# Kernel optimization log

Hardware: AMD Instinct MI355X
Metric: run time of the kernel (lower is better)

## Reference

```python
import jax, jax.numpy as jnp
import numpy as np

DIM = 256
FEATURE_SCALE = 4
NMS_THRESHOLD = 8.0
PRE_NMS_TOPK = 2048
MAX_OUTPUT = 256
MIN_SCORE = 0.2


def conv3d_same(x, w, b):
    # x: [D,H,W,Cin], w: [3,3,3,Cin,Cout] -> [D,H,W,Cout], SAME padding (flax default)
    y = jax.lax.conv_general_dilated(
        x[None], w, window_strides=(1, 1, 1), padding="SAME",
        dimension_numbers=("NDHWC", "DHWIO", "NDHWC"))
    return y[0] + b


def setup_inputs() -> dict:
    key = jax.random.key(0)
    ks = jax.random.split(key, 8)
    D, H, W, C = 16, 64, 64, 256
    feature = jax.random.normal(ks[0], (D, H, W, C), jnp.float32)
    mask = jax.random.bernoulli(ks[1], 0.8, (D * FEATURE_SCALE, H * FEATURE_SCALE, W * FEATURE_SCALE))
    s3a = 1.0 / np.sqrt(27 * C)
    s3b = 1.0 / np.sqrt(27 * DIM)
    s1 = 1.0 / np.sqrt(DIM)
    w0 = jax.random.normal(ks[2], (3, 3, 3, C, DIM), jnp.float32) * s3a
    b0 = jnp.zeros((DIM,), jnp.float32)
    w1 = jax.random.normal(ks[3], (3, 3, 3, DIM, DIM), jnp.float32) * s3b
    b1 = jnp.zeros((DIM,), jnp.float32)
    w_logit = jax.random.normal(ks[4], (DIM, 1), jnp.float32) * s1
    b_logit = jnp.zeros((1,), jnp.float32)
    w_reg = jax.random.normal(ks[5], (DIM, 3), jnp.float32) * s1
    b_reg = jnp.zeros((3,), jnp.float32)
    return dict(feature=feature, mask=mask, w0=w0, b0=b0, w1=w1, b1=b1,
                w_logit=w_logit, b_logit=b_logit, w_reg=w_reg, b_reg=b_reg)


def reference(feature, mask, w0, b0, w1, b1, w_logit, b_logit, w_reg, b_reg):
    # ---- feature mixing: n_layers=2 of conv3d + gelu (flax gelu is approximate/tanh) ----
    x = jax.nn.gelu(conv3d_same(feature, w0, b0))
    x = jax.nn.gelu(conv3d_same(x, w1, b1))
    D, H, W = x.shape[:3]

    # ---- detection block: 1x1 convs are pointwise dense layers ----
    logits = (x @ w_logit + b_logit)[..., 0].reshape(-1)          # [N]
    regressions = (x @ w_reg + b_reg)                              # [D,H,W,3]
    ref_locs = (jnp.moveaxis(jnp.mgrid[:D, :H, :W], 0, -1) + 0.5) * FEATURE_SCALE
    pred_locs = (ref_locs + regressions * FEATURE_SCALE).reshape(-1, 3)  # [N,3]

    # ---- generate_predictions: sigmoid scores, pre-NMS top-k, greedy distance NMS ----
    scores = jax.nn.sigmoid(logits)
    top_scores, idx = jax.lax.top_k(scores, PRE_NMS_TOPK)          # sorted desc
    top_locs = pred_locs[idx]                                      # [K,3]
    d2 = ((top_locs[:, None, :] - top_locs[None, :, :]) ** 2).sum(-1)  # [K,K]
    th2 = NMS_THRESHOLD * NMS_THRESHOLD

    def step(suppressed, i):
        keep_i = (~suppressed[i]) & (top_scores[i] >= MIN_SCORE)
        suppressed = suppressed | (keep_i & (d2[i] < th2))
        return suppressed, keep_i

    _, keep = jax.lax.scan(step, jnp.zeros((PRE_NMS_TOPK,), bool), jnp.arange(PRE_NMS_TOPK))
    sel_scores = jnp.where(keep, top_scores, 0.0)
    out_scores, oidx = jax.lax.top_k(sel_scores, MAX_OUTPUT)       # [M]
    out_locs = top_locs[oidx]                                      # [M,3]

    # ---- mask gather: floor/clip/index, zero out-of-mask scores ----
    pli = jnp.floor(out_locs).astype(jnp.int32)
    bound = jnp.array(mask.shape, jnp.int32) - 1
    plc = jnp.clip(pli, 0, bound)
    in_range = (pli == plc).all(axis=1)
    masked = jnp.where(in_range, mask[plc[:, 0], plc[:, 1], plc[:, 2]], False)
    out_scores = jnp.where(masked, out_scores, 0.0)

    return jnp.concatenate([out_locs, out_scores[:, None]], axis=-1)  # [M,4] = (z,y,x,score)
```

## Files before the change

### kernel.cpp

```cpp
#include <hip/hip_runtime.h>
#include <math.h>

#define Dz 16
#define Hy 64
#define Wx 64
#define CHN 256
#define NVOX (Dz*Hy*Wx)
#define TOPK 2048
#define MAXOUT 256
#define CAND_CAP 4096
#define NBCAP 16
#define NHIST 65536

typedef __attribute__((ext_vector_type(8))) _Float16 h8;
typedef __attribute__((ext_vector_type(8))) unsigned short u16x8;
typedef __attribute__((ext_vector_type(4))) float f32x4;

__device__ __forceinline__ float gelu_tanh(float x) {
    return 0.5f*x*(1.0f + tanhf(0.7978845608028654f*(x + 0.044715f*x*x*x)));
}
__device__ __forceinline__ unsigned f2sort(float f) {
    unsigned u = __float_as_uint(f);
    return (u & 0x80000000u) ? ~u : (u | 0x80000000u);
}
__device__ __forceinline__ float sort2f(unsigned s) {
    unsigned u = (s & 0x80000000u) ? (s & 0x7fffffffu) : ~s;
    return __uint_as_float(u);
}

#define MFMA(d, a, b) d = __builtin_amdgcn_mfma_f32_16x16x32_f16(a, b, d, 0, 0, 0)

__device__ __forceinline__ void gl_lds16(const void* g, void* l) {
    __builtin_amdgcn_global_load_lds(
        (const __attribute__((address_space(1))) void*)g,
        (__attribute__((address_space(3))) void*)l, 16, 0, 0);
}

__global__ __launch_bounds__(256) void prep_kernel(const float* __restrict__ w0,
        const float* __restrict__ w1, u16x8* __restrict__ wpk0,
        u16x8* __restrict__ wpk1, unsigned* __restrict__ hist,
        unsigned* __restrict__ counter, float4* __restrict__ zerob) {
    int b = blockIdx.x, t = threadIdx.x;
    if (b < 1728) {
        int id = b*256 + t;
        int l = (id >= 221184) ? 1 : 0;
        int r = id - l*221184;
        int lane = r & 63, ng = (r >> 6) & 15, kbg = (r >> 10) & 7, tp = r >> 13;
        const float* w = l ? w1 : w0;
        u16x8* dst = l ? wpk1 : wpk0;
        h8 hv, lv;
        #pragma unroll
        for (int j = 0; j < 8; ++j) {
            int k = kbg*32 + (lane >> 4)*8 + j;
            int co = ng*16 + (lane & 15);
            float v = w[((size_t)tp*CHN + k)*CHN + co];
            _Float16 h = (_Float16)v;
            hv[j] = h;
            lv[j] = (_Float16)(v - (float)h);
        }
        size_t base = (((size_t)(tp*8 + kbg)*16 + ng)*2)*64 + lane;
        dst[base]      = __builtin_bit_cast(u16x8, hv);
        dst[base + 64] = __builtin_bit_cast(u16x8, lv);
    } else {
        int zb = b - 1728;
        int i = zb*256 + t;
        hist[i] = 0u; hist[i + 16384] = 0u; hist[i + 32768] = 0u; hist[i + 49152] = 0u;
        if (zb == 0 && t == 0) counter[0] = 0u;
        if (zb == 0 && t == 2) *zerob = make_float4(0.f, 0.f, 0.f, 0.f);
    }
}

template<int LAYER>
__device__ __forceinline__ void stage_chunk(int cidx, void* ldst,
        const float* f32in, const unsigned short* hhi, const unsigned short* hlo,
        const float4* zerob, int zz, bool zok, int y0, int kc) {
    const void* src;
    if (LAYER == 0) {
        int c = cidx & 15, rr = cidx >> 4;
        int r = rr % 66, iy = rr / 66;
        int ygl = y0 - 1 + iy, xin = r - 1;
        bool ok = zok & ((unsigned)ygl < (unsigned)Hy) & ((unsigned)xin < (unsigned)Wx);
        int cs = c ^ ((r & 7) << 1);
        src = ok ? (const void*)(f32in + ((size_t)(((size_t)zz*Hy + ygl)*Wx + xin))*CHN
                                 + kc*64 + cs*4)
                 : (const void*)zerob;
    } else {
        int c = cidx & 7, rr = cidx >> 3;
        int r = rr % 66, tt = rr / 66;
        int p = tt >> 2, iy = tt & 3;
        int ygl = y0 - 1 + iy, xin = r - 1;
        bool ok = zok & ((unsigned)ygl < (unsigned)Hy) & ((unsigned)xin < (unsigned)Wx);
        int cs = c ^ (r & 7);
        const unsigned short* bp = p ? hlo : hhi;
        src = ok ? (const void*)(bp + ((size_t)(((size_t)zz*Hy + ygl)*Wx + xin))*CHN
                                 + kc*64 + cs*8)
                 : (const void*)zerob;
    }
    gl_lds16(src, ldst);
}

template<int LAYER>
__global__ __launch_bounds__(512, 4) void conv_kernel(
        const float* __restrict__ f32in,
        const unsigned short* __restrict__ hhi, const unsigned short* __restrict__ hlo,
        const u16x8* __restrict__ wpk, const float* __restrict__ bias,
        const float4* __restrict__ zerob,
        unsigned short* __restrict__ ohi, unsigned short* __restrict__ olo,
        const float* __restrict__ wlog, const float* __restrict__ blog,
        const float* __restrict__ wreg, const float* __restrict__ breg,
        float* __restrict__ locs, unsigned long long* __restrict__ keys,
        unsigned* __restrict__ hist) {
    __shared__ h8 sm[4224];
    const int tid = threadIdx.x;
    const int lane = tid & 63, w = tid >> 6;
    const int yo = w >> 2, wn = w & 3;
    const int lr = lane & 15, lg = lane >> 4;
    const int z = blockIdx.y, y0 = blockIdx.x*2;
    const int wbs = tid & ~63;

    f32x4 acc[4][4];
    #pragma unroll
    for (int m = 0; m < 4; ++m)
        #pragma unroll
        for (int n = 0; n < 4; ++n) acc[m][n] = (f32x4){0.f,0.f,0.f,0.f};

    for (int dz = 0; dz < 3; ++dz) {
        const int zz = z + dz - 1;
        const bool zok = (unsigned)zz < (unsigned)Dz;
        for (int kc = 0; kc < 4; ++kc) {
            __syncthreads();
            #pragma unroll
            for (int k = 0; k < 8; ++k)
                stage_chunk<LAYER>(k*512 + tid, (void*)&sm[k*512 + wbs],
                                   f32in, hhi, hlo, zerob, zz, zok, y0, kc);
            if (tid < 128)
                stage_chunk<LAYER>(4096 + tid, (void*)&sm[4096 + wbs],
                                   f32in, hhi, hlo, zerob, zz, zok, y0, kc);
            asm volatile("s_waitcnt vmcnt(0)" ::: "memory");
            __syncthreads();
            for (int dy = 0; dy < 3; ++dy) {
                const int iyA = yo + dy;
                #pragma unroll
                for (int dx = 0; dx < 3; ++dx) {
                    const int tap = (dz*3 + dy)*3 + dx;
                    #pragma unroll
                    for (int kb = 0; kb < 2; ++kb) {
                        const int kbg = kc*2 + kb;
                        const u16x8* wb = wpk + ((size_t)(tap*8 + kbg)*32 + wn*8)*64 + lane;
                        h8 bh[4];
                        #pragma unroll
                        for (int n = 0; n < 4; ++n)
                            bh[n] = __builtin_bit_cast(h8, wb[(size_t)n*128]);
                        #pragma unroll
                        for (int m = 0; m < 4; ++m) {
                            const int r = m*16 + lr + dx;
                            h8 ah, al;
                            if (LAYER == 0) {
                                const f32x4* Af = (const f32x4*)sm + ((size_t)iyA*66 + r)*16;
                                int s0 = (kb*8 + lg*2) ^ ((r & 7) << 1);
                                f32x4 a0 = Af[s0], a1 = Af[s0 | 1];
                                #pragma unroll
                                for (int j = 0; j < 4; ++j) {
                                    _Float16 h0 = (_Float16)a0[j];
                                    ah[j] = h0; al[j] = (_Float16)(a0[j] - (float)h0);
                                    _Float16 h1 = (_Float16)a1[j];
                                    ah[4+j] = h1; al[4+j] = (_Float16)(a1[j] - (float)h1);
                                }
                            } else {
                                const int sl = (kb*4 + lg) ^ (r & 7);
                                ah = sm[((size_t)iyA*66 + r)*8 + sl];
                                al = sm[2112 + ((size_t)iyA*66 + r)*8 + sl];
                            }
                            #pragma unroll
                            for (int n = 0; n < 4; ++n) {
                                MFMA(acc[m][n], ah, bh[n]);
                                MFMA(acc[m][n], al, bh[n]);
                            }
                        }
                        h8 bl[4];
                        #pragma unroll
                        for (int n = 0; n < 4; ++n)
                            bl[n] = __builtin_bit_cast(h8, wb[(size_t)n*128 + 64]);
                        #pragma unroll
                        for (int m = 0; m < 4; ++m) {
                            const int r = m*16 + lr + dx;
                            h8 ah;
                            if (LAYER == 0) {
                                const f32x4* Af = (const f32x4*)sm + ((size_t)iyA*66 + r)*16;
                                int s0 = (kb*8 + lg*2) ^ ((r & 7) << 1);
                                f32x4 a0 = Af[s0], a1 = Af[s0 | 1];
                                #pragma unroll
                                for (int j = 0; j < 4; ++j) {
                                    ah[j] = (_Float16)a0[j];
                                    ah[4+j] = (_Float16)a1[j];
                                }
                            } else {
                                const int sl = (kb*4 + lg) ^ (r & 7);
                                ah = sm[((size_t)iyA*66 + r)*8 + sl];
                            }
                            #pragma unroll
                            for (int n = 0; n < 4; ++n) MFMA(acc[m][n], ah, bl[n]);
                        }
                    }
                }
            }
        }
    }

    float bn[4];
    #pragma unroll
    for (int n = 0; n < 4; ++n) bn[n] = bias[wn*64 + n*16 + lr];

    if (LAYER == 0) {
        const int ygl = y0 + yo;
        #pragma unroll
        for (int m = 0; m < 4; ++m) {
            #pragma unroll
            for (int rg = 0; rg < 4; ++rg) {
                const int x = m*16 + lg*4 + rg;
                const size_t vbase = ((size_t)((z*Hy + ygl)*Wx + x))*CHN;
                #pragma unroll
                for (int n = 0; n < 4; ++n) {
                    const int co = wn*64 + n*16 + lr;
                    float g = gelu_tanh(acc[m][n][rg] + bn[n]);
                    _Float16 h = (_Float16)g;
                    _Float16 l = (_Float16)(g - (float)h);
                    ohi[vbase + co] = __builtin_bit_cast(unsigned short, h);
                    olo[vbase + co] = __builtin_bit_cast(unsigned short, l);
                }
            }
        }
    } else {
        float wl[4], wr0[4], wr1[4], wr2[4];
        #pragma unroll
        for (int n = 0; n < 4; ++n) {
            const int co = wn*64 + n*16 + lr;
            wl[n] = wlog[co];
            wr0[n] = wreg[co*3 + 0]; wr1[n] = wreg[co*3 + 1]; wr2[n] = wreg[co*3 + 2];
        }
        float p[4][16];
        #pragma unroll
        for (int c = 0; c < 4; ++c)
            #pragma unroll
            for (int xi = 0; xi < 16; ++xi) p[c][xi] = 0.f;
        #pragma unroll
        for (int m = 0; m < 4; ++m)
            #pragma unroll
            for (int rg = 0; rg < 4; ++rg) {
                const int xi = m*4 + rg;
                #pragma unroll
                for (int n = 0; n < 4; ++n) {
                    float g = gelu_tanh(acc[m][n][rg] + bn[n]);
                    p[0][xi] += g*wl[n];
                    p[1][xi] += g*wr0[n];
                    p[2][xi] += g*wr1[n];
                    p[3][xi] += g*wr2[n];
                }
            }
        #pragma unroll
        for (int st = 0; st < 4; ++st) {
            const int s = 1 << st;
            #pragma unroll
            for (int c = 0; c < 4; ++c)
                #pragma unroll
                for (int xi = 0; xi < 16; ++xi)
                    p[c][xi] += __shfl_xor(p[c][xi], s, 64);
        }
        __syncthreads();
        float* det = (float*)sm;
        if (lr == 0) {
            #pragma unroll
            for (int m = 0; m < 4; ++m)
                #pragma unroll
                for (int rg = 0; rg < 4; ++rg) {
                    const int x = m*16 + lg*4 + rg;
                    #pragma unroll
                    for (int c = 0; c < 4; ++c)
                        det[((yo*64 + x)*4 + c)*4 + wn] = p[c][m*4 + rg];
                }
        }
        __syncthreads();
        {
            const int yo2 = tid >> 8, x = (tid >> 2) & 63, chn = tid & 3;
            const float* dp = det + ((yo2*64 + x)*4 + chn)*4;
            float s = dp[0] + dp[1] + dp[2] + dp[3];
            const int ygl = y0 + yo2;
            const int vg = (z*Hy + ygl)*Wx + x;
            if (chn == 0) {
                float logit = s + blog[0];
                float score = 1.f/(1.f + expf(-logit));
                unsigned sb = f2sort(score);
                keys[vg] = ((unsigned long long)sb << 32)
                         | (unsigned long long)(0xFFFFFFFFu - (unsigned)vg);
                atomicAdd(&hist[sb >> 16], 1u);
            } else {
                float coord = (chn == 1) ? (float)z : (chn == 2) ? (float)ygl : (float)x;
                float loc = (coord + 0.5f)*4.0f + (s + breg[chn-1])*4.0f;
                locs[(size_t)vg*3 + (chn-1)] = loc;
            }
        }
    }
}

__global__ __launch_bounds__(1024) void find_cut_kernel(const unsigned* __restrict__ hist,
                                                        unsigned* __restrict__ cutp) {
    __shared__ unsigned ps[1024];
    __shared__ unsigned fs[64];
    __shared__ int sh_cb;
    __shared__ unsigned sh_acc;
    int t = threadIdx.x;
    unsigned s = 0;
    const unsigned* hp = hist + (size_t)t*64;
    for (int j = 0; j < 64; ++j) s += hp[j];
    ps[t] = s;
    __syncthreads();
    for (int off = 1; off < 1024; off <<= 1) {
        unsigned v = ps[t] + ((t + off < 1024) ? ps[t + off] : 0u);
        __syncthreads();
        ps[t] = v;
        __syncthreads();
    }
    if (ps[t] >= TOPK && (t == 1023 || ps[t+1] < TOPK)) {
        sh_cb = t; sh_acc = (t == 1023) ? 0u : ps[t+1];
    }
    __syncthreads();
    int cb = sh_cb; unsigned acc = sh_acc;
    if (t < 64) {
        unsigned f = acc;
        for (int u = t; u < 64; ++u) f += hist[(size_t)cb*64 + u];
        fs[t] = f;
    }
    __syncthreads();
    if (t < 64) {
        if (fs[t] >= TOPK && (t == 63 || fs[t+1] < TOPK))
            cutp[0] = ((unsigned)(cb*64 + t)) << 16;
    }
}

__global__ void compact_kernel(const unsigned long long* __restrict__ keys,
                               const unsigned* __restrict__ cutp,
                               unsigned* __restrict__ counter,
                               unsigned long long* __restrict__ cand) {
    int i = blockIdx.x*blockDim.x + threadIdx.x;
    unsigned thr = cutp[0];
    unsigned long long k = keys[i];
    if ((unsigned)(k >> 32) >= thr) {
        unsigned p = atomicAdd(counter, 1u);
        if (p < CAND_CAP) cand[p] = k;
    }
}

__global__ __launch_bounds__(128) void rank_kernel(const unsigned* __restrict__ counter,
        const unsigned long long* __restrict__ cand, const float* __restrict__ locs,
        float4* __restrict__ loc4G) {
    __shared__ unsigned long long kbuf[CAND_CAP];
    int t = threadIdx.x;
    int g = blockIdx.x*128 + t;
    int M = (int)*counter; if (M > CAND_CAP) M = CAND_CAP;
    for (int i = t; i < CAND_CAP; i += 128) kbuf[i] = (i < M) ? cand[i] : 0ull;
    __syncthreads();
    if (g >= M) return;
    unsigned long long mykey = kbuf[g];
    int rank = 0;
    for (int j = 0; j < M; ++j) rank += (kbuf[j] > mykey) ? 1 : 0;
    if (rank < TOPK) {
        unsigned idx = 0xFFFFFFFFu - (unsigned)(mykey & 0xFFFFFFFFull);
        float4 v;
        v.x = locs[(size_t)idx*3 + 0];
        v.y = locs[(size_t)idx*3 + 1];
        v.z = locs[(size_t)idx*3 + 2];
        v.w = sort2f((unsigned)(mykey >> 32));
        loc4G[rank] = v;
    }
}

__global__ __launch_bounds__(64) void nbr_kernel(const float4* __restrict__ loc4G,
        unsigned short* __restrict__ nbidx, unsigned char* __restrict__ nbcnt) {
    __shared__ float4 b4[TOPK];
    int t = threadIdx.x;
    int g = blockIdx.x*64 + t;
    for (int i = t; i < TOPK; i += 64) b4[i] = loc4G[i];
    __syncthreads();
    float4 me = b4[g];
    int cnt = 0;
    for (int j = 0; j < TOPK; ++j) {
        float4 o = b4[j];
        float dz = o.x - me.x, dy = o.y - me.y, dx = o.z - me.z;
        float d2 = dz*dz + dy*dy + dx*dx;
        if (d2 < 64.0f && j != g) {
            if (cnt < NBCAP) nbidx[(size_t)g*NBCAP + cnt] = (unsigned short)j;
            cnt++;
        }
    }
    nbcnt[g] = (unsigned char)min(cnt, 255);
}

__global__ __launch_bounds__(512) void nms_kernel(const float4* __restrict__ loc4G,
        const unsigned short* __restrict__ nbidx, const unsigned char* __restrict__ nbcnt,
        const int* __restrict__ mask, float* __restrict__ out) {
    __shared__ float4 p4[TOPK];
    __shared__ unsigned short snb[TOPK*NBCAP];
    __shared__ unsigned char scnt[TOPK];
    __shared__ unsigned char supf[TOPK];
    __shared__ unsigned char keepB[TOPK];
    __shared__ unsigned keepw[64];
    __shared__ int wpre[64];
    __shared__ int sh_nk;
    int t = threadIdx.x;
    for (int i = t; i < TOPK; i += 512) {
        p4[i] = loc4G[i]; scnt[i] = nbcnt[i]; supf[i] = 0; keepB[i] = 0;
    }
    for (int i = t; i < TOPK*NBCAP/8; i += 512)
        ((uint4*)snb)[i] = ((const uint4*)nbidx)[i];
    __syncthreads();
    if (t < 64) {
        const int l = t;
        float cz[32], cy[32], cx[32];
        #pragma unroll
        for (int j = 0; j < 32; ++j) {
            float4 v = p4[l*32 + j];
            cz[j] = v.x; cy[j] = v.y; cx[j] = v.z;
        }
        int myok = 0;
        #pragma unroll
        for (int j = 0; j < 32; ++j) myok += (p4[l*32 + j].w >= 0.2f) ? 1 : 0;
        #pragma unroll
        for (int s = 1; s < 64; s <<= 1) myok += __shfl_xor(myok, s, 64);
        const int NS = myok;
        int keeps = 0;
        for (int i = 0; i < NS; ++i) {
            bool kept = (supf[i] == 0);
            if (kept) {
                if (l == 0) keepB[i] = 1;
                ++keeps;
                const int cnt = scnt[i];
                if (cnt <= NBCAP) {
                    if (l < cnt) supf[snb[i*NBCAP + l]] = 1;
                } else {
                    float4 pv = p4[i];
                    #pragma unroll
                    for (int j = 0; j < 32; ++j) {
                        float dz = cz[j]-pv.x, dy = cy[j]-pv.y, dx = cx[j]-pv.z;
                        if (dz*dz + dy*dy + dx*dx < 64.0f) supf[l*32 + j] = 1;
                    }
                }
                asm volatile("s_waitcnt lgkmcnt(0)" ::: "memory");
                if (keeps >= MAXOUT) break;
            }
        }
    }
    __syncthreads();
    if (t < 64) {
        unsigned wmask = 0u;
        for (int j = 0; j < 32; ++j) wmask |= (keepB[t*32 + j] ? 1u : 0u) << j;
        keepw[t] = wmask;
    }
    __syncthreads();
    if (t < 64) {
        int p = 0;
        for (int j = 0; j < t; ++j) p += __popc(keepw[j]);
        wpre[t] = p;
        if (t == 63) sh_nk = p + __popc(keepw[63]);
    }
    __syncthreads();
    const int nk = sh_nk;
    for (int i = t; i < TOPK; i += 512) {
        unsigned w = keepw[i >> 5];
        bool kp = (w >> (i & 31)) & 1u;
        int rk = wpre[i >> 5] + __popc(w & ((1u << (i & 31)) - 1u));
        int slot = kp ? rk : (nk + (i - rk));
        if (slot < MAXOUT) {
            float4 v = p4[i];
            float lz = v.x, ly = v.y, lx = v.z;
            float sc = kp ? v.w : 0.f;
            int iz = (int)floorf(lz), iy = (int)floorf(ly), ix = (int)floorf(lx);
            int cz2 = min(max(iz,0),Dz*4-1), cy2 = min(max(iy,0),Hy*4-1), cx2 = min(max(ix,0),Wx*4-1);
            bool inr = (iz==cz2) && (iy==cy2) && (ix==cx2);
            float osc = (inr && mask[((size_t)cz2*(Hy*4) + cy2)*(Wx*4) + cx2] != 0) ? sc : 0.f;
            out[slot*4+0] = lz; out[slot*4+1] = ly; out[slot*4+2] = lx; out[slot*4+3] = osc;
        }
    }
}

extern "C" void kernel_launch(void* const* d_in, const int* in_sizes, int n_in,
                              void* d_out, int out_size, void* d_ws, size_t ws_size,
                              hipStream_t stream) {
    const float* feature = (const float*)d_in[0];
    const int*   mask    = (const int*)d_in[1];
    const float* w0   = (const float*)d_in[2];
    const float* b0   = (const float*)d_in[3];
    const float* w1   = (const float*)d_in[4];
    const float* b1   = (const float*)d_in[5];
    const float* wlog = (const float*)d_in[6];
    const float* blog = (const float*)d_in[7];
    const float* wreg = (const float*)d_in[8];
    const float* breg = (const float*)d_in[9];

    char* ws = (char*)d_ws;
    size_t off = 0;
    unsigned short* h1hi = (unsigned short*)(ws + off); off += (size_t)NVOX*CHN*2;
    unsigned short* h1lo = (unsigned short*)(ws + off); off += (size_t)NVOX*CHN*2;
    u16x8* wpk0 = (u16x8*)(ws + off);               off += (size_t)442368*16;
    u16x8* wpk1 = (u16x8*)(ws + off);               off += (size_t)442368*16;
    unsigned long long* keys = (unsigned long long*)(ws + off); off += (size_t)NVOX*8;
    float* locs = (float*)(ws + off);               off += (size_t)NVOX*3*4;
    unsigned* hist = (unsigned*)(ws + off);         off += (size_t)NHIST*4;
    unsigned* counter = (unsigned*)(ws + off);      off += 256;
    unsigned* cutp = counter + 1;
    float4* zerob = (float4*)(ws + off);            off += 256;
    unsigned long long* cand = (unsigned long long*)(ws + off); off += (size_t)CAND_CAP*8;
    float4* loc4G = (float4*)(ws + off);            off += (size_t)TOPK*16;
    unsigned short* nbidx = (unsigned short*)(ws + off); off += (size_t)TOPK*NBCAP*2;
    unsigned char* nbcnt = (unsigned char*)(ws + off);   off += (size_t)TOPK;
    if (ws_size < off) return;

    prep_kernel<<<1792, 256, 0, stream>>>(w0, w1, wpk0, wpk1, hist, counter, zerob);
    dim3 cgrid(Hy/2, Dz);
    conv_kernel<0><<<cgrid, 512, 0, stream>>>(feature, nullptr, nullptr, wpk0, b0,
                                              zerob, h1hi, h1lo,
                                              nullptr, nullptr, nullptr, nullptr,
                                              nullptr, nullptr, nullptr);
    conv_kernel<1><<<cgrid, 512, 0, stream>>>(nullptr, h1hi, h1lo, wpk1, b1,
                                              zerob, nullptr, nullptr,
                                              wlog, blog, wreg, breg,
                                              locs, keys, hist);
    find_cut_kernel<<<1, 1024, 0, stream>>>(hist, cutp);
    compact_kernel<<<NVOX/256, 256, 0, stream>>>(keys, cutp, counter, cand);
    rank_kernel<<<CAND_CAP/128, 128, 0, stream>>>(counter, cand, locs, loc4G);
    nbr_kernel<<<TOPK/64, 64, 0, stream>>>(loc4G, nbidx, nbcnt);
    nms_kernel<<<1, 512, 0, stream>>>(loc4G, nbidx, nbcnt, mask, (float*)d_out);
}
```

Before: 1.560 ms.

## Stage conv tiles via register loads and pre-split fp32 input into fp16 hi/lo

Replaces the direct global-to-LDS async loads with ordinary global loads into registers, then stores to shared memory with zero-fill for padding, which removes the need for the zero buffer. For layer 0 the fp32 input is split into fp16 hi/lo once during staging, so it is no longer reconverted for every tap and column in the inner MFMA loop. This cuts redundant conversion ALU work and lets both layers share one LDS read path. The cost is losing the async direct-to-LDS copy, so staging now goes through VGPRs and may add register pressure and latency.

```diff
diff --git a/kernel.cpp b/kernel.cpp
--- a/kernel.cpp
+++ b/kernel.cpp
@@ -30,16 +30,10 @@
 
 #define MFMA(d, a, b) d = __builtin_amdgcn_mfma_f32_16x16x32_f16(a, b, d, 0, 0, 0)
 
-__device__ __forceinline__ void gl_lds16(const void* g, void* l) {
-    __builtin_amdgcn_global_load_lds(
-        (const __attribute__((address_space(1))) void*)g,
-        (__attribute__((address_space(3))) void*)l, 16, 0, 0);
-}
-
 __global__ __launch_bounds__(256) void prep_kernel(const float* __restrict__ w0,
         const float* __restrict__ w1, u16x8* __restrict__ wpk0,
         u16x8* __restrict__ wpk1, unsigned* __restrict__ hist,
-        unsigned* __restrict__ counter, float4* __restrict__ zerob) {
+        unsigned* __restrict__ counter) {
     int b = blockIdx.x, t = threadIdx.x;
     if (b < 1728) {
         int id = b*256 + t;
@@ -66,45 +60,14 @@
         int i = zb*256 + t;
         hist[i] = 0u; hist[i + 16384] = 0u; hist[i + 32768] = 0u; hist[i + 49152] = 0u;
         if (zb == 0 && t == 0) counter[0] = 0u;
-        if (zb == 0 && t == 2) *zerob = make_float4(0.f, 0.f, 0.f, 0.f);
-    }
-}
-
-template<int LAYER>
-__device__ __forceinline__ void stage_chunk(int cidx, void* ldst,
-        const float* f32in, const unsigned short* hhi, const unsigned short* hlo,
-        const float4* zerob, int zz, bool zok, int y0, int kc) {
-    const void* src;
-    if (LAYER == 0) {
-        int c = cidx & 15, rr = cidx >> 4;
-        int r = rr % 66, iy = rr / 66;
-        int ygl = y0 - 1 + iy, xin = r - 1;
-        bool ok = zok & ((unsigned)ygl < (unsigned)Hy) & ((unsigned)xin < (unsigned)Wx);
-        int cs = c ^ ((r & 7) << 1);
-        src = ok ? (const void*)(f32in + ((size_t)(((size_t)zz*Hy + ygl)*Wx + xin))*CHN
-                                 + kc*64 + cs*4)
-                 : (const void*)zerob;
-    } else {
-        int c = cidx & 7, rr = cidx >> 3;
-        int r = rr % 66, tt = rr / 66;
-        int p = tt >> 2, iy = tt & 3;
-        int ygl = y0 - 1 + iy, xin = r - 1;
-        bool ok = zok & ((unsigned)ygl < (unsigned)Hy) & ((unsigned)xin < (unsigned)Wx);
-        int cs = c ^ (r & 7);
-        const unsigned short* bp = p ? hlo : hhi;
-        src = ok ? (const void*)(bp + ((size_t)(((size_t)zz*Hy + ygl)*Wx + xin))*CHN
-                                 + kc*64 + cs*8)
-                 : (const void*)zerob;
-    }
-    gl_lds16(src, ldst);
+    }
 }
 
 template<int LAYER>
 __global__ __launch_bounds__(512, 4) void conv_kernel(
-        const float* __restrict__ f32in,
+        const float* __restrict__ fsrc,
         const unsigned short* __restrict__ hhi, const unsigned short* __restrict__ hlo,
         const u16x8* __restrict__ wpk, const float* __restrict__ bias,
-        const float4* __restrict__ zerob,
         unsigned short* __restrict__ ohi, unsigned short* __restrict__ olo,
         const float* __restrict__ wlog, const float* __restrict__ blog,
         const float* __restrict__ wreg, const float* __restrict__ breg,
@@ -116,7 +79,6 @@
     const int yo = w >> 2, wn = w & 3;
     const int lr = lane & 15, lg = lane >> 4;
     const int z = blockIdx.y, y0 = blockIdx.x*2;
-    const int wbs = tid & ~63;
 
     f32x4 acc[4][4];
     #pragma unroll
@@ -126,20 +88,54 @@
 
     for (int dz = 0; dz < 3; ++dz) {
         const int zz = z + dz - 1;
-        const bool zok = (unsigned)zz < (unsigned)Dz;
         for (int kc = 0; kc < 4; ++kc) {
             __syncthreads();
-            #pragma unroll
-            for (int k = 0; k < 8; ++k)
-                stage_chunk<LAYER>(k*512 + tid, (void*)&sm[k*512 + wbs],
-                                   f32in, hhi, hlo, zerob, zz, zok, y0, kc);
-            if (tid < 128)
-                stage_chunk<LAYER>(4096 + tid, (void*)&sm[4096 + wbs],
-                                   f32in, hhi, hlo, zerob, zz, zok, y0, kc);
-            asm volatile("s_waitcnt vmcnt(0)" ::: "memory");
+            if (LAYER == 0) {
+                for (int cidx = tid; cidx < 2112; cidx += 512) {
+                    int cd = cidx & 7;
+                    int rr = cidx >> 3;
+                    int r = rr % 66, iy = rr / 66;
+                    int ygl = y0 - 1 + iy, xin = r - 1;
+                    h8 hv = {0,0,0,0,0,0,0,0}, lv = {0,0,0,0,0,0,0,0};
+                    if (((unsigned)zz < (unsigned)Dz) & ((unsigned)ygl < (unsigned)Hy)
+                        & ((unsigned)xin < (unsigned)Wx)) {
+                        const float* s = fsrc + ((size_t)((zz*Hy + ygl)*Wx + xin))*CHN
+                                              + kc*64 + cd*8;
+                        float4 t0 = *(const float4*)s;
+                        float4 t1 = *(const float4*)(s + 4);
+                        float vv[8] = {t0.x,t0.y,t0.z,t0.w,t1.x,t1.y,t1.z,t1.w};
+                        #pragma unroll
+                        for (int j = 0; j < 8; ++j) {
+                            _Float16 h = (_Float16)vv[j];
+                            hv[j] = h;
+                            lv[j] = (_Float16)(vv[j] - (float)h);
+                        }
+                    }
+                    int sl = cd ^ (r & 7);
+                    sm[(iy*66 + r)*8 + sl] = hv;
+                    sm[2112 + (iy*66 + r)*8 + sl] = lv;
+                }
+            } else {
+                for (int cidx = tid; cidx < 4224; cidx += 512) {
+                    int c = cidx & 7;
+                    int rr = cidx >> 3;
+                    int r = rr % 66, tt = rr / 66;
+                    int p = tt >> 2, iy = tt & 3;
+                    int ygl = y0 - 1 + iy, xin = r - 1;
+                    u16x8 v = {0,0,0,0,0,0,0,0};
+                    if (((unsigned)zz < (unsigned)Dz) & ((unsigned)ygl < (unsigned)Hy)
+                        & ((unsigned)xin < (unsigned)Wx)) {
+                        const unsigned short* bp = p ? hlo : hhi;
+                        v = *(const u16x8*)(bp + ((size_t)((zz*Hy + ygl)*Wx + xin))*CHN
+                                               + kc*64 + (size_t)((c ^ (r & 7)))*8);
+                    }
+                    sm[cidx] = __builtin_bit_cast(h8, v);
+                }
+            }
             __syncthreads();
             for (int dy = 0; dy < 3; ++dy) {
                 const int iyA = yo + dy;
+                const h8* As = sm + iyA*528;
                 #pragma unroll
                 for (int dx = 0; dx < 3; ++dx) {
                     const int tap = (dz*3 + dy)*3 + dx;
@@ -154,23 +150,9 @@
                         #pragma unroll
                         for (int m = 0; m < 4; ++m) {
                             const int r = m*16 + lr + dx;
-                            h8 ah, al;
-                            if (LAYER == 0) {
-                                const f32x4* Af = (const f32x4*)sm + ((size_t)iyA*66 + r)*16;
-                                int s0 = (kb*8 + lg*2) ^ ((r & 7) << 1);
-                                f32x4 a0 = Af[s0], a1 = Af[s0 | 1];
-                                #pragma unroll
-                                for (int j = 0; j < 4; ++j) {
-                                    _Float16 h0 = (_Float16)a0[j];
-                                    ah[j] = h0; al[j] = (_Float16)(a0[j] - (float)h0);
-                                    _Float16 h1 = (_Float16)a1[j];
-                                    ah[4+j] = h1; al[4+j] = (_Float16)(a1[j] - (float)h1);
-                                }
-                            } else {
-                                const int sl = (kb*4 + lg) ^ (r & 7);
-                                ah = sm[((size_t)iyA*66 + r)*8 + sl];
-                                al = sm[2112 + ((size_t)iyA*66 + r)*8 + sl];
-                            }
+                            const int sl = (kb*4 + lg) ^ (r & 7);
+                            h8 ah = As[r*8 + sl];
+                            h8 al = As[2112 + r*8 + sl];
                             #pragma unroll
                             for (int n = 0; n < 4; ++n) {
                                 MFMA(acc[m][n], ah, bh[n]);
@@ -184,20 +166,8 @@
                         #pragma unroll
                         for (int m = 0; m < 4; ++m) {
                             const int r = m*16 + lr + dx;
-                            h8 ah;
-                            if (LAYER == 0) {
-                                const f32x4* Af = (const f32x4*)sm + ((size_t)iyA*66 + r)*16;
-                                int s0 = (kb*8 + lg*2) ^ ((r & 7) << 1);
-                                f32x4 a0 = Af[s0], a1 = Af[s0 | 1];
-                                #pragma unroll
-                                for (int j = 0; j < 4; ++j) {
-                                    ah[j] = (_Float16)a0[j];
-                                    ah[4+j] = (_Float16)a1[j];
-                                }
-                            } else {
-                                const int sl = (kb*4 + lg) ^ (r & 7);
-                                ah = sm[((size_t)iyA*66 + r)*8 + sl];
-                            }
+                            const int sl = (kb*4 + lg) ^ (r & 7);
+                            h8 ah = As[r*8 + sl];
                             #pragma unroll
                             for (int n = 0; n < 4; ++n) MFMA(acc[m][n], ah, bl[n]);
                         }
@@ -507,21 +477,20 @@
     unsigned* hist = (unsigned*)(ws + off);         off += (size_t)NHIST*4;
     unsigned* counter = (unsigned*)(ws + off);      off += 256;
     unsigned* cutp = counter + 1;
-    float4* zerob = (float4*)(ws + off);            off += 256;
     unsigned long long* cand = (unsigned long long*)(ws + off); off += (size_t)CAND_CAP*8;
     float4* loc4G = (float4*)(ws + off);            off += (size_t)TOPK*16;
     unsigned short* nbidx = (unsigned short*)(ws + off); off += (size_t)TOPK*NBCAP*2;
     unsigned char* nbcnt = (unsigned char*)(ws + off);   off += (size_t)TOPK;
     if (ws_size < off) return;
 
-    prep_kernel<<<1792, 256, 0, stream>>>(w0, w1, wpk0, wpk1, hist, counter, zerob);
+    prep_kernel<<<1792, 256, 0, stream>>>(w0, w1, wpk0, wpk1, hist, counter);
     dim3 cgrid(Hy/2, Dz);
     conv_kernel<0><<<cgrid, 512, 0, stream>>>(feature, nullptr, nullptr, wpk0, b0,
-                                              zerob, h1hi, h1lo,
+                                              h1hi, h1lo,
                                               nullptr, nullptr, nullptr, nullptr,
                                               nullptr, nullptr, nullptr);
     conv_kernel<1><<<cgrid, 512, 0, stream>>>(nullptr, h1hi, h1lo, wpk1, b1,
-                                              zerob, nullptr, nullptr,
+                                              nullptr, nullptr,
                                               wlog, blog, wreg, breg,
                                               locs, keys, hist);
     find_cut_kernel<<<1, 1024, 0, stream>>>(hist, cutp);
```

Result: faster. 1.382 ms (-11.4%).
